# Kernel optimization log

Hardware: AMD Instinct MI355X
Metric: run time of the kernel (lower is better)

## Reference

```python
import jax, jax.numpy as jnp
import numpy as np

FG_THRESH = 0.5
BG_THRESH_HI = 0.5
BG_THRESH_LO = 0.1


def _bbox_overlaps(boxes, query):
    x1 = jnp.maximum(boxes[:, None, 0], query[None, :, 0])
    y1 = jnp.maximum(boxes[:, None, 1], query[None, :, 1])
    x2 = jnp.minimum(boxes[:, None, 2], query[None, :, 2])
    y2 = jnp.minimum(boxes[:, None, 3], query[None, :, 3])
    iw = jnp.clip(x2 - x1 + 1.0, 0.0)
    ih = jnp.clip(y2 - y1 + 1.0, 0.0)
    inter = iw * ih  # [N,C]
    area_b = (boxes[:, 2] - boxes[:, 0] + 1.0) * (boxes[:, 3] - boxes[:, 1] + 1.0)
    area_q = (query[:, 2] - query[:, 0] + 1.0) * (query[:, 3] - query[:, 1] + 1.0)
    return inter / (area_b[:, None] + area_q[None, :] - inter)


def _refine_supervision(prob, ss_boxes, pos_mask, IS_weight):
    # vectorized, fully on-device version of get_refine_supervision
    C = pos_mask.shape[0]
    p = jax.lax.stop_gradient(prob * IS_weight)  # original detaches via .data.cpu().numpy()
    if p.shape[1] == C + 1:
        p = p[:, 1:]  # drop background column
    max_idx = jnp.argmax(p, axis=0)                     # [C] top-scoring roi per class
    boxes_c = jax.lax.stop_gradient(ss_boxes)[max_idx, 1:5]  # [C,4] pseudo-GT boxes
    ov = _bbox_overlaps(jax.lax.stop_gradient(ss_boxes)[:, 1:5], boxes_c)  # [N,C]
    ov = jnp.where(pos_mask[None, :], ov, -1.0)         # only image-level positive classes
    gt = jnp.argmax(ov, axis=1)                         # [N] assignment
    mo = jnp.max(ov, axis=1)                            # [N] max overlap
    fg = mo > FG_THRESH
    bg = (mo >= BG_THRESH_LO) & (mo < BG_THRESH_HI)
    keep = fg | bg                                      # keep_inds as a mask
    col = jnp.where(fg, gt + 1, 0)                      # one-hot column per kept roi
    return keep, col


def _refine_loss(refine_prob, keep, col, IS_weight):
    n = jnp.sum(keep).astype(refine_prob.dtype)
    lp = jnp.take_along_axis(jnp.log(refine_prob), col[:, None], axis=1)[:, 0]  # [N]
    return -jnp.sum(jnp.where(keep, IS_weight[:, 0] * lp, 0.0)) / n


def reference(fc7_roi, fc7_context, fc7_frame, W_cls, b_cls, W_det, b_det,
              W_r1, b_r1, W_r2, b_r2, ss_boxes, IS_weight, image_level_label):
    C = W_cls.shape[1]
    cls_score = fc7_roi @ W_cls + b_cls                       # [N,C]
    det_score = (fc7_frame @ W_det + b_det) - (fc7_context @ W_det + b_det)  # frame - context
    refine_prob_1 = jax.nn.softmax(fc7_roi @ W_r1 + b_r1, axis=1)  # [N,C+1]
    refine_prob_2 = jax.nn.softmax(fc7_roi @ W_r2 + b_r2, axis=1)
    cls_prob = jax.nn.softmax(cls_score, axis=1)
    det_prob = jax.nn.softmax(det_score, axis=0)              # softmax over rois
    det_cls_prob_product = cls_prob * det_prob                # [N,C]
    det_cls_score = jnp.sum(cls_score * det_prob, axis=0)     # [C]

    pos_mask = image_level_label[0] == 1                      # [C]
    keep1, col1 = _refine_supervision(det_cls_prob_product, ss_boxes, pos_mask, IS_weight)
    refine_loss_1 = _refine_loss(refine_prob_1, keep1, col1, IS_weight)
    keep2, col2 = _refine_supervision(refine_prob_1, ss_boxes, pos_mask, IS_weight)
    refine_loss_2 = _refine_loss(refine_prob_2, keep2, col2, IS_weight)

    lab = image_level_label[0].astype(det_cls_score.dtype)    # +/-1 labels
    cls_det_loss = jnp.sum(jnp.maximum(0.0, 1.0 - lab * det_cls_score)) / C
    total_loss = cls_det_loss + 0.1 * refine_loss_1 + 0.1 * refine_loss_2
    return total_loss


def setup_inputs() -> dict:
    key = jax.random.key(0)
    ks = jax.random.split(key, 16)
    N, F, C = 4096, 4096, 20
    s = 0.01  # weight scale to keep softmax/hinge well-conditioned
    fc7_roi = jax.random.normal(ks[0], (N, F), jnp.float32)
    fc7_context = jax.random.normal(ks[1], (N, F), jnp.float32)
    fc7_frame = jax.random.normal(ks[2], (N, F), jnp.float32)
    W_cls = jax.random.normal(ks[3], (F, C), jnp.float32) * s
    W_det = jax.random.normal(ks[4], (F, C), jnp.float32) * s
    W_r1 = jax.random.normal(ks[5], (F, C + 1), jnp.float32) * s
    W_r2 = jax.random.normal(ks[6], (F, C + 1), jnp.float32) * s
    b_cls = jnp.zeros((C,), jnp.float32)
    b_det = jnp.zeros((C,), jnp.float32)
    b_r1 = jnp.zeros((C + 1,), jnp.float32)
    b_r2 = jnp.zeros((C + 1,), jnp.float32)
    x1 = jax.random.uniform(ks[7], (N,), jnp.float32, 0.0, 500.0)
    y1 = jax.random.uniform(ks[8], (N,), jnp.float32, 0.0, 500.0)
    w = jax.random.uniform(ks[9], (N,), jnp.float32, 10.0, 120.0)
    h = jax.random.uniform(ks[10], (N,), jnp.float32, 10.0, 120.0)
    ss_boxes = jnp.stack([jnp.zeros((N,), jnp.float32), x1, y1, x1 + w, y1 + h], axis=1)
    IS_weight = jax.random.uniform(ks[11], (N, 1), jnp.float32, 0.5, 1.0)
    lbl = jnp.where(jax.random.bernoulli(ks[12], 0.4, (1, C)), 1, -1).astype(jnp.int32)
    lbl = lbl.at[0, 0].set(1)  # guarantee at least one positive class
    return {"fc7_roi": fc7_roi, "fc7_context": fc7_context, "fc7_frame": fc7_frame,
            "W_cls": W_cls, "b_cls": b_cls, "W_det": W_det, "b_det": b_det,
            "W_r1": W_r1, "b_r1": b_r1, "W_r2": W_r2, "b_r2": b_r2,
            "ss_boxes": ss_boxes, "IS_weight": IS_weight, "image_level_label": lbl}
```

## Files before the change

### kernel.cpp

```cpp
#include <hip/hip_runtime.h>

typedef __attribute__((ext_vector_type(4))) float f32x4;
typedef __attribute__((ext_vector_type(8))) short short8;

#define N_ROWS 4096
#define KDIM   4096
#define NC     96
#define NSPLIT 16

__device__ inline short f2bf(float f) {
  unsigned u = __builtin_bit_cast(unsigned, f);
  u += 0x7FFFu + ((u >> 16) & 1u);
  return (short)(u >> 16);
}

__global__ void k_pack(const float* __restrict__ Wcls, const float* __restrict__ Wr1,
                       const float* __restrict__ Wr2, const float* __restrict__ Wdet,
                       ushort* __restrict__ Wp) {
  int t = blockIdx.x * 256 + threadIdx.x;
  int ks = t / 3072;
  int rem = t - ks * 3072;
  int ct = rem >> 9;
  int rem2 = rem & 511;
  int l = rem2 >> 3;
  int j = rem2 & 7;
  int k = ks * 32 + (l >> 4) * 8 + j;
  int col = ct * 16 + (l & 15);
  float v = 0.f;
  if (col < 20)                 v = Wcls[k * 20 + col];
  else if (col < 41)            v = Wr1[k * 21 + (col - 20)];
  else if (col < 62)            v = Wr2[k * 21 + (col - 41)];
  else if (col >= 64 && col < 84) v = Wdet[k * 20 + (col - 64)];
  Wp[t] = (ushort)f2bf(v);
}

__global__ __launch_bounds__(256) void k_gemm(const float* __restrict__ roi,
    const float* __restrict__ frame, const float* __restrict__ ctx,
    const ushort* __restrict__ Wp, float* __restrict__ Spart) {
  const int lane = threadIdx.x & 63;
  const int wid = blockIdx.x * 4 + (threadIdx.x >> 6);
  const int rt = wid & 255;
  const int ks = wid >> 8;
  const int row = rt * 16 + (lane & 15);
  const int kg = lane >> 4;
  const float* pr = roi   + (size_t)row * KDIM;
  const float* pf = frame + (size_t)row * KDIM;
  const float* pc = ctx   + (size_t)row * KDIM;
  f32x4 acc[6];
#pragma unroll
  for (int i = 0; i < 6; ++i) acc[i] = (f32x4){0.f, 0.f, 0.f, 0.f};
  const int s0 = ks * 8;
  for (int s = 0; s < 8; ++s) {
    const int kk = (s0 + s) * 32 + kg * 8;
    f32x4 r0 = *(const f32x4*)(pr + kk);
    f32x4 r1 = *(const f32x4*)(pr + kk + 4);
    f32x4 f0 = *(const f32x4*)(pf + kk);
    f32x4 f1 = *(const f32x4*)(pf + kk + 4);
    f32x4 c0 = *(const f32x4*)(pc + kk);
    f32x4 c1 = *(const f32x4*)(pc + kk + 4);
    short8 aR, aD;
#pragma unroll
    for (int j = 0; j < 4; ++j) {
      aR[j]     = f2bf(r0[j]);
      aR[j + 4] = f2bf(r1[j]);
      aD[j]     = f2bf(f0[j] - c0[j]);
      aD[j + 4] = f2bf(f1[j] - c1[j]);
    }
    const ushort* wb = Wp + ((size_t)(s0 + s) * 6) * 512 + lane * 8;
#pragma unroll
    for (int ct = 0; ct < 6; ++ct) {
      short8 b = *(const short8*)(wb + ct * 512);
      acc[ct] = __builtin_amdgcn_mfma_f32_16x16x32_bf16(ct < 4 ? aR : aD, b, acc[ct], 0, 0, 0);
    }
  }
  float* out = Spart + (size_t)ks * (N_ROWS * NC) + (size_t)rt * 16 * NC;
  const int rbase = (lane >> 4) * 4;
  const int col = lane & 15;
#pragma unroll
  for (int ct = 0; ct < 6; ++ct)
#pragma unroll
    for (int r = 0; r < 4; ++r)
      out[(size_t)(rbase + r) * NC + ct * 16 + col] = acc[ct][r];
}

__global__ void k_reduce(const float* __restrict__ Spart, float* __restrict__ S) {
  int e = blockIdx.x * 256 + threadIdx.x;
  float s = 0.f;
#pragma unroll
  for (int ks = 0; ks < NSPLIT; ++ks) s += Spart[(size_t)ks * (N_ROWS * NC) + e];
  S[e] = s;
}

__global__ void k_rows(const float* __restrict__ S, const float* __restrict__ bcls,
    const float* __restrict__ br1, const float* __restrict__ br2,
    float* __restrict__ clsp, float* __restrict__ rp1,
    float* __restrict__ lse1, float* __restrict__ lse2) {
  int i = blockIdx.x * 256 + threadIdx.x;
  const float* sr = S + (size_t)i * NC;
  float s[21];
  float m = -3.4e38f;
  for (int c = 0; c < 20; ++c) { s[c] = sr[c] + bcls[c]; m = fmaxf(m, s[c]); }
  float sum = 0.f;
  for (int c = 0; c < 20; ++c) { float e = expf(s[c] - m); s[c] = e; sum += e; }
  float inv = 1.f / sum;
  for (int c = 0; c < 20; ++c) clsp[(size_t)i * 20 + c] = s[c] * inv;
  m = -3.4e38f;
  for (int c = 0; c < 21; ++c) { s[c] = sr[20 + c] + br1[c]; m = fmaxf(m, s[c]); }
  sum = 0.f;
  for (int c = 0; c < 21; ++c) { float e = expf(s[c] - m); s[c] = e; sum += e; }
  lse1[i] = m + logf(sum);
  inv = 1.f / sum;
  for (int c = 0; c < 21; ++c) rp1[(size_t)i * 21 + c] = s[c] * inv;
  m = -3.4e38f;
  for (int c = 0; c < 21; ++c) { s[c] = sr[41 + c] + br2[c]; m = fmaxf(m, s[c]); }
  sum = 0.f;
  for (int c = 0; c < 21; ++c) sum += expf(s[c] - m);
  lse2[i] = m + logf(sum);
}

__global__ __launch_bounds__(256) void k_col(const float* __restrict__ S,
    const float* __restrict__ clsp, const float* __restrict__ rp1,
    const float* __restrict__ isw, const float* __restrict__ ssb,
    const float* __restrict__ bcls,
    float* __restrict__ dcs, float* __restrict__ b1out, float* __restrict__ b2out) {
  const int c = blockIdx.x;
  const int t = threadIdx.x;
  __shared__ float rv[256];
  __shared__ int ri[256];
  float m = -3.4e38f;
  for (int i = t; i < N_ROWS; i += 256) m = fmaxf(m, S[(size_t)i * NC + 64 + c]);
  rv[t] = m; __syncthreads();
  for (int o = 128; o; o >>= 1) { if (t < o) rv[t] = fmaxf(rv[t], rv[t + o]); __syncthreads(); }
  const float M = rv[0]; __syncthreads();
  float se = 0.f, scd = 0.f, v1b = -3.4e38f, v2b = -3.4e38f;
  int i1 = 0, i2 = 0;
  for (int i = t; i < N_ROWS; i += 256) {
    float w = isw[i];
    float e = expf(S[(size_t)i * NC + 64 + c] - M);
    se += e;
    scd += (S[(size_t)i * NC + c] + bcls[c]) * e;
    float v1 = clsp[(size_t)i * 20 + c] * e * w;
    if (v1 > v1b) { v1b = v1; i1 = i; }
    float v2 = rp1[(size_t)i * 21 + c + 1] * w;
    if (v2 > v2b) { v2b = v2; i2 = i; }
  }
  rv[t] = se; __syncthreads();
  for (int o = 128; o; o >>= 1) { if (t < o) rv[t] += rv[t + o]; __syncthreads(); }
  const float SE = rv[0]; __syncthreads();
  rv[t] = scd; __syncthreads();
  for (int o = 128; o; o >>= 1) { if (t < o) rv[t] += rv[t + o]; __syncthreads(); }
  const float SCD = rv[0]; __syncthreads();
  rv[t] = v1b; ri[t] = i1; __syncthreads();
  for (int o = 128; o; o >>= 1) {
    if (t < o) { if (rv[t + o] > rv[t] || (rv[t + o] == rv[t] && ri[t + o] < ri[t])) { rv[t] = rv[t + o]; ri[t] = ri[t + o]; } }
    __syncthreads();
  }
  const int I1 = ri[0]; __syncthreads();
  rv[t] = v2b; ri[t] = i2; __syncthreads();
  for (int o = 128; o; o >>= 1) {
    if (t < o) { if (rv[t + o] > rv[t] || (rv[t + o] == rv[t] && ri[t + o] < ri[t])) { rv[t] = rv[t + o]; ri[t] = ri[t + o]; } }
    __syncthreads();
  }
  const int I2 = ri[0];
  if (t == 0) {
    dcs[c] = SCD / SE;
    for (int q = 0; q < 4; ++q) {
      b1out[c * 4 + q] = ssb[(size_t)I1 * 5 + 1 + q];
      b2out[c * 4 + q] = ssb[(size_t)I2 * 5 + 1 + q];
    }
  }
}

__global__ __launch_bounds__(256) void k_sup(const float* __restrict__ S,
    const float* __restrict__ ssb, const float* __restrict__ isw,
    const int* __restrict__ label,
    const float* __restrict__ b1in, const float* __restrict__ b2in,
    const float* __restrict__ lse1, const float* __restrict__ lse2,
    const float* __restrict__ br1, const float* __restrict__ br2,
    float* __restrict__ scal) {
  __shared__ float q1[20][4], q2[20][4], a1[20], a2[20];
  __shared__ int pos[20];
  const int t = threadIdx.x;
  if (t < 20) {
    for (int q = 0; q < 4; ++q) { q1[t][q] = b1in[t * 4 + q]; q2[t][q] = b2in[t * 4 + q]; }
    a1[t] = (q1[t][2] - q1[t][0] + 1.f) * (q1[t][3] - q1[t][1] + 1.f);
    a2[t] = (q2[t][2] - q2[t][0] + 1.f) * (q2[t][3] - q2[t][1] + 1.f);
    pos[t] = (label[t] == 1);
  }
  __syncthreads();
  const int i = blockIdx.x * 256 + t;
  const float bx1 = ssb[(size_t)i * 5 + 1], by1 = ssb[(size_t)i * 5 + 2];
  const float bx2 = ssb[(size_t)i * 5 + 3], by2 = ssb[(size_t)i * 5 + 4];
  const float ab = (bx2 - bx1 + 1.f) * (by2 - by1 + 1.f);
  const float w = isw[i];
  float p1 = 0.f, n1 = 0.f, p2 = 0.f, n2 = 0.f;
  {
    float mo = -2.f; int gt = 0;
    for (int c = 0; c < 20; ++c) {
      float v = -1.f;
      if (pos[c]) {
        float xx1 = fmaxf(bx1, q1[c][0]), yy1 = fmaxf(by1, q1[c][1]);
        float xx2 = fminf(bx2, q1[c][2]), yy2 = fminf(by2, q1[c][3]);
        float iw = fmaxf(xx2 - xx1 + 1.f, 0.f), ih = fmaxf(yy2 - yy1 + 1.f, 0.f);
        float inter = iw * ih;
        v = inter / (ab + a1[c] - inter);
      }
      if (v > mo) { mo = v; gt = c; }
    }
    bool fg = mo > 0.5f;
    bool bg = (mo >= 0.1f) && (mo < 0.5f);
    if (fg || bg) {
      int col = fg ? gt + 1 : 0;
      float lp = S[(size_t)i * NC + 20 + col] + br1[col] - lse1[i];
      p1 = w * lp; n1 = 1.f;
    }
  }
  {
    float mo = -2.f; int gt = 0;
    for (int c = 0; c < 20; ++c) {
      float v = -1.f;
      if (pos[c]) {
        float xx1 = fmaxf(bx1, q2[c][0]), yy1 = fmaxf(by1, q2[c][1]);
        float xx2 = fminf(bx2, q2[c][2]), yy2 = fminf(by2, q2[c][3]);
        float iw = fmaxf(xx2 - xx1 + 1.f, 0.f), ih = fmaxf(yy2 - yy1 + 1.f, 0.f);
        float inter = iw * ih;
        v = inter / (ab + a2[c] - inter);
      }
      if (v > mo) { mo = v; gt = c; }
    }
    bool fg = mo > 0.5f;
    bool bg = (mo >= 0.1f) && (mo < 0.5f);
    if (fg || bg) {
      int col = fg ? gt + 1 : 0;
      float lp = S[(size_t)i * NC + 41 + col] + br2[col] - lse2[i];
      p2 = w * lp; n2 = 1.f;
    }
  }
  __shared__ float rs[256];
  float sums[4] = {p1, n1, p2, n2};
  float tot[4];
  for (int q = 0; q < 4; ++q) {
    rs[t] = sums[q]; __syncthreads();
    for (int o = 128; o; o >>= 1) { if (t < o) rs[t] += rs[t + o]; __syncthreads(); }
    tot[q] = rs[0]; __syncthreads();
  }
  if (t == 0) {
    atomicAdd(&scal[0], tot[0]); atomicAdd(&scal[1], tot[1]);
    atomicAdd(&scal[2], tot[2]); atomicAdd(&scal[3], tot[3]);
  }
}

__global__ void k_final(const float* __restrict__ dcs, const int* __restrict__ label,
                        const float* __restrict__ scal, float* __restrict__ out) {
  if (threadIdx.x == 0 && blockIdx.x == 0) {
    float cd = 0.f;
    for (int c = 0; c < 20; ++c) {
      float lab = (float)label[c];
      cd += fmaxf(1.f - lab * dcs[c], 0.f);
    }
    cd *= (1.f / 20.f);
    float rl1 = -scal[0] / scal[1];
    float rl2 = -scal[2] / scal[3];
    out[0] = cd + 0.1f * (rl1 + rl2);
  }
}

constexpr size_t OFF_S     = 0;
constexpr size_t OFF_SCAL  = OFF_S + (size_t)N_ROWS * NC * 4;
constexpr size_t OFF_DCS   = OFF_SCAL + 16;
constexpr size_t OFF_B1    = OFF_DCS + 80;
constexpr size_t OFF_B2    = OFF_B1 + 320;
constexpr size_t OFF_LSE1  = OFF_B2 + 320;
constexpr size_t OFF_LSE2  = OFF_LSE1 + 16384;
constexpr size_t OFF_CLSP  = OFF_LSE2 + 16384;
constexpr size_t OFF_RP1   = OFF_CLSP + 327680;
constexpr size_t OFF_WP    = OFF_RP1 + 344064;
constexpr size_t OFF_SPART = OFF_WP + 786432;

extern "C" void kernel_launch(void* const* d_in, const int* in_sizes, int n_in,
                              void* d_out, int out_size, void* d_ws, size_t ws_size,
                              hipStream_t stream) {
  const float* roi   = (const float*)d_in[0];
  const float* ctx   = (const float*)d_in[1];
  const float* frame = (const float*)d_in[2];
  const float* Wcls  = (const float*)d_in[3];
  const float* bcls  = (const float*)d_in[4];
  const float* Wdet  = (const float*)d_in[5];
  const float* Wr1   = (const float*)d_in[7];
  const float* br1   = (const float*)d_in[8];
  const float* Wr2   = (const float*)d_in[9];
  const float* br2   = (const float*)d_in[10];
  const float* ssb   = (const float*)d_in[11];
  const float* isw   = (const float*)d_in[12];
  const int*   label = (const int*)d_in[13];

  char* ws = (char*)d_ws;
  float*  S     = (float*)(ws + OFF_S);
  float*  scal  = (float*)(ws + OFF_SCAL);
  float*  dcs   = (float*)(ws + OFF_DCS);
  float*  b1    = (float*)(ws + OFF_B1);
  float*  b2    = (float*)(ws + OFF_B2);
  float*  lse1  = (float*)(ws + OFF_LSE1);
  float*  lse2  = (float*)(ws + OFF_LSE2);
  float*  clsp  = (float*)(ws + OFF_CLSP);
  float*  rp1   = (float*)(ws + OFF_RP1);
  ushort* Wp    = (ushort*)(ws + OFF_WP);
  float*  Spart = (float*)(ws + OFF_SPART);

  hipMemsetAsync(scal, 0, 16, stream);
  k_pack<<<1536, 256, 0, stream>>>(Wcls, Wr1, Wr2, Wdet, Wp);
  k_gemm<<<1024, 256, 0, stream>>>(roi, frame, ctx, Wp, Spart);
  k_reduce<<<1536, 256, 0, stream>>>(Spart, S);
  k_rows<<<16, 256, 0, stream>>>(S, bcls, br1, br2, clsp, rp1, lse1, lse2);
  k_col<<<20, 256, 0, stream>>>(S, clsp, rp1, isw, ssb, bcls, dcs, b1, b2);
  k_sup<<<16, 256, 0, stream>>>(S, ssb, isw, label, b1, b2, lse1, lse2, br1, br2, scal);
  k_final<<<1, 64, 0, stream>>>(dcs, label, scal, (float*)d_out);
}
```

Measured before the change: 96.03 us.

## Pipeline GEMM A loads with triple buffering, stage B in LDS, fuse reduce+rows

```diff
diff --git a/kernel.cpp b/kernel.cpp
--- a/kernel.cpp
+++ b/kernel.cpp
@@ -2,11 +2,12 @@
 
 typedef __attribute__((ext_vector_type(4))) float f32x4;
 typedef __attribute__((ext_vector_type(8))) short short8;
+typedef __attribute__((ext_vector_type(4))) unsigned int u32x4;
 
 #define N_ROWS 4096
 #define KDIM   4096
 #define NC     96
-#define NSPLIT 16
+#define GSPLIT 16
 
 __device__ inline short f2bf(float f) {
   unsigned u = __builtin_bit_cast(unsigned, f);
@@ -14,17 +15,23 @@
   return (short)(u >> 16);
 }
 
+__device__ inline unsigned cvtpk(float lo, float hi) {
+  unsigned r;
+  asm("v_cvt_pk_bf16_f32 %0, %1, %2" : "=v"(r) : "v"(lo), "v"(hi));
+  return r;
+}
+
 __global__ void k_pack(const float* __restrict__ Wcls, const float* __restrict__ Wr1,
                        const float* __restrict__ Wr2, const float* __restrict__ Wdet,
                        ushort* __restrict__ Wp) {
   int t = blockIdx.x * 256 + threadIdx.x;
-  int ks = t / 3072;
-  int rem = t - ks * 3072;
+  int K = t / 3072;
+  int rem = t - K * 3072;
   int ct = rem >> 9;
   int rem2 = rem & 511;
   int l = rem2 >> 3;
   int j = rem2 & 7;
-  int k = ks * 32 + (l >> 4) * 8 + j;
+  int k = K * 32 + (l >> 4) * 8 + j;
   int col = ct * 16 + (l & 15);
   float v = 0.f;
   if (col < 20)                 v = Wcls[k * 20 + col];
@@ -34,46 +41,79 @@
   Wp[t] = (ushort)f2bf(v);
 }
 
-__global__ __launch_bounds__(256) void k_gemm(const float* __restrict__ roi,
+#define GLo(dst, base, OFF) \
+  asm volatile("global_load_dwordx4 %0, %1, off offset:%c2" : "=v"(dst) : "v"(base), "i"(OFF) : "memory")
+#define WAITV(N) asm volatile("s_waitcnt vmcnt(" #N ")" ::: "memory")
+#define SB() __builtin_amdgcn_sched_barrier(0)
+
+#define ISSUEA(KS, BF) do {                              \
+    GLo(raw[BF][0], pr, (KS)*128);                       \
+    GLo(raw[BF][1], pr, (KS)*128 + 16);                  \
+    GLo(raw[BF][2], pf, (KS)*128);                       \
+    GLo(raw[BF][3], pf, (KS)*128 + 16);                  \
+    GLo(raw[BF][4], pc, (KS)*128);                       \
+    GLo(raw[BF][5], pc, (KS)*128 + 16);                  \
+  } while (0)
+
+__global__ __launch_bounds__(256, 3) void k_gemm(const float* __restrict__ roi,
     const float* __restrict__ frame, const float* __restrict__ ctx,
     const ushort* __restrict__ Wp, float* __restrict__ Spart) {
-  const int lane = threadIdx.x & 63;
-  const int wid = blockIdx.x * 4 + (threadIdx.x >> 6);
-  const int rt = wid & 255;
-  const int ks = wid >> 8;
-  const int row = rt * 16 + (lane & 15);
-  const int kg = lane >> 4;
-  const float* pr = roi   + (size_t)row * KDIM;
-  const float* pf = frame + (size_t)row * KDIM;
-  const float* pc = ctx   + (size_t)row * KDIM;
+  const int t    = threadIdx.x;
+  const int lane = t & 63;
+  const int wid  = t >> 6;
+  const int rb   = blockIdx.x >> 4;
+  const int g    = blockIdx.x & 15;
+
+  __shared__ alignas(16) ushort smemB[8 * 6 * 64 * 8];
+
+  {
+    const ushort* src = Wp + (size_t)g * 24576;
+    for (int r = 0; r < 12; ++r) {
+      const int e = r * 256 + t;
+      *(short8*)(&smemB[e * 8]) = *(const short8*)(src + e * 8);
+    }
+  }
+  __syncthreads();
+
+  const int row = rb * 64 + wid * 16 + (lane & 15);
+  const size_t aoff = (size_t)row * KDIM + g * 256 + (lane >> 4) * 8;
+  const float* pr = roi   + aoff;
+  const float* pf = frame + aoff;
+  const float* pc = ctx   + aoff;
+
+  f32x4 raw[3][6];
   f32x4 acc[6];
 #pragma unroll
   for (int i = 0; i < 6; ++i) acc[i] = (f32x4){0.f, 0.f, 0.f, 0.f};
-  const int s0 = ks * 8;
-  for (int s = 0; s < 8; ++s) {
-    const int kk = (s0 + s) * 32 + kg * 8;
-    f32x4 r0 = *(const f32x4*)(pr + kk);
-    f32x4 r1 = *(const f32x4*)(pr + kk + 4);
-    f32x4 f0 = *(const f32x4*)(pf + kk);
-    f32x4 f1 = *(const f32x4*)(pf + kk + 4);
-    f32x4 c0 = *(const f32x4*)(pc + kk);
-    f32x4 c1 = *(const f32x4*)(pc + kk + 4);
-    short8 aR, aD;
-#pragma unroll
-    for (int j = 0; j < 4; ++j) {
-      aR[j]     = f2bf(r0[j]);
-      aR[j + 4] = f2bf(r1[j]);
-      aD[j]     = f2bf(f0[j] - c0[j]);
-      aD[j + 4] = f2bf(f1[j] - c1[j]);
-    }
-    const ushort* wb = Wp + ((size_t)(s0 + s) * 6) * 512 + lane * 8;
+
+  ISSUEA(0, 0);
+  ISSUEA(1, 1);
+
+#pragma unroll
+  for (int ks = 0; ks < 8; ++ks) {
+    if (ks < 6) ISSUEA(ks + 2, (ks + 2) % 3);
+    if (ks < 6)      { WAITV(12); }
+    else if (ks == 6){ WAITV(6); }
+    else             { WAITV(0); }
+    SB();
+    const f32x4* c = raw[ks % 3];
+    u32x4 uR, uD;
+    uR.x = cvtpk(c[0][0], c[0][1]); uR.y = cvtpk(c[0][2], c[0][3]);
+    uR.z = cvtpk(c[1][0], c[1][1]); uR.w = cvtpk(c[1][2], c[1][3]);
+    uD.x = cvtpk(c[2][0] - c[4][0], c[2][1] - c[4][1]);
+    uD.y = cvtpk(c[2][2] - c[4][2], c[2][3] - c[4][3]);
+    uD.z = cvtpk(c[3][0] - c[5][0], c[3][1] - c[5][1]);
+    uD.w = cvtpk(c[3][2] - c[5][2], c[3][3] - c[5][3]);
+    const short8 aR = __builtin_bit_cast(short8, uR);
+    const short8 aD = __builtin_bit_cast(short8, uD);
 #pragma unroll
     for (int ct = 0; ct < 6; ++ct) {
-      short8 b = *(const short8*)(wb + ct * 512);
+      const short8 b = *(const short8*)(&smemB[((ks * 6 + ct) * 64 + lane) * 8]);
       acc[ct] = __builtin_amdgcn_mfma_f32_16x16x32_bf16(ct < 4 ? aR : aD, b, acc[ct], 0, 0, 0);
     }
   }
-  float* out = Spart + (size_t)ks * (N_ROWS * NC) + (size_t)rt * 16 * NC;
+
+  float* out = Spart + (size_t)g * (N_ROWS * NC) + (size_t)(rb * 64 + wid * 16) * NC;
   const int rbase = (lane >> 4) * 4;
   const int col = lane & 15;
 #pragma unroll
@@ -83,39 +123,45 @@
       out[(size_t)(rbase + r) * NC + ct * 16 + col] = acc[ct][r];
 }
 
-__global__ void k_reduce(const float* __restrict__ Spart, float* __restrict__ S) {
-  int e = blockIdx.x * 256 + threadIdx.x;
-  float s = 0.f;
-#pragma unroll
-  for (int ks = 0; ks < NSPLIT; ++ks) s += Spart[(size_t)ks * (N_ROWS * NC) + e];
-  S[e] = s;
-}
-
-__global__ void k_rows(const float* __restrict__ S, const float* __restrict__ bcls,
+__global__ void k_rr(const float* __restrict__ Spart, const float* __restrict__ bcls,
     const float* __restrict__ br1, const float* __restrict__ br2,
-    float* __restrict__ clsp, float* __restrict__ rp1,
+    float* __restrict__ S, float* __restrict__ clsp, float* __restrict__ rp1,
     float* __restrict__ lse1, float* __restrict__ lse2) {
-  int i = blockIdx.x * 256 + threadIdx.x;
-  const float* sr = S + (size_t)i * NC;
-  float s[21];
-  float m = -3.4e38f;
-  for (int c = 0; c < 20; ++c) { s[c] = sr[c] + bcls[c]; m = fmaxf(m, s[c]); }
-  float sum = 0.f;
-  for (int c = 0; c < 20; ++c) { float e = expf(s[c] - m); s[c] = e; sum += e; }
-  float inv = 1.f / sum;
-  for (int c = 0; c < 20; ++c) clsp[(size_t)i * 20 + c] = s[c] * inv;
-  m = -3.4e38f;
-  for (int c = 0; c < 21; ++c) { s[c] = sr[20 + c] + br1[c]; m = fmaxf(m, s[c]); }
-  sum = 0.f;
-  for (int c = 0; c < 21; ++c) { float e = expf(s[c] - m); s[c] = e; sum += e; }
-  lse1[i] = m + logf(sum);
-  inv = 1.f / sum;
-  for (int c = 0; c < 21; ++c) rp1[(size_t)i * 21 + c] = s[c] * inv;
-  m = -3.4e38f;
-  for (int c = 0; c < 21; ++c) { s[c] = sr[41 + c] + br2[c]; m = fmaxf(m, s[c]); }
-  sum = 0.f;
-  for (int c = 0; c < 21; ++c) sum += expf(s[c] - m);
-  lse2[i] = m + logf(sum);
+  const int b = blockIdx.x;
+  const int t = threadIdx.x;
+  const int base = b * 3072;
+#pragma unroll
+  for (int j = 0; j < 12; ++j) {
+    const int e = base + j * 256 + t;
+    float s = 0.f;
+#pragma unroll
+    for (int gg = 0; gg < GSPLIT; ++gg) s += Spart[(size_t)gg * (N_ROWS * NC) + e];
+    S[e] = s;
+  }
+  __syncthreads();
+  if (t < 32) {
+    const int i = b * 32 + t;
+    const float* sr = S + (size_t)i * NC;
+    float s[21];
+    float m = -3.4e38f;
+    for (int c = 0; c < 20; ++c) { s[c] = sr[c] + bcls[c]; m = fmaxf(m, s[c]); }
+    float sum = 0.f;
+    for (int c = 0; c < 20; ++c) { float e = expf(s[c] - m); s[c] = e; sum += e; }
+    float inv = 1.f / sum;
+    for (int c = 0; c < 20; ++c) clsp[(size_t)i * 20 + c] = s[c] * inv;
+    m = -3.4e38f;
+    for (int c = 0; c < 21; ++c) { s[c] = sr[20 + c] + br1[c]; m = fmaxf(m, s[c]); }
+    sum = 0.f;
+    for (int c = 0; c < 21; ++c) { float e = expf(s[c] - m); s[c] = e; sum += e; }
+    lse1[i] = m + logf(sum);
+    inv = 1.f / sum;
+    for (int c = 0; c < 21; ++c) rp1[(size_t)i * 21 + c] = s[c] * inv;
+    m = -3.4e38f;
+    for (int c = 0; c < 21; ++c) { s[c] = sr[41 + c] + br2[c]; m = fmaxf(m, s[c]); }
+    sum = 0.f;
+    for (int c = 0; c < 21; ++c) sum += expf(s[c] - m);
+    lse2[i] = m + logf(sum);
+  }
 }
 
 __global__ __launch_bounds__(256) void k_col(const float* __restrict__ S,
@@ -310,8 +356,7 @@
   hipMemsetAsync(scal, 0, 16, stream);
   k_pack<<<1536, 256, 0, stream>>>(Wcls, Wr1, Wr2, Wdet, Wp);
   k_gemm<<<1024, 256, 0, stream>>>(roi, frame, ctx, Wp, Spart);
-  k_reduce<<<1536, 256, 0, stream>>>(Spart, S);
-  k_rows<<<16, 256, 0, stream>>>(S, bcls, br1, br2, clsp, rp1, lse1, lse2);
+  k_rr<<<128, 256, 0, stream>>>(Spart, bcls, br1, br2, S, clsp, rp1, lse1, lse2);
   k_col<<<20, 256, 0, stream>>>(S, clsp, rp1, isw, ssb, bcls, dcs, b1, b2);
   k_sup<<<16, 256, 0, stream>>>(S, ssb, isw, label, b1, b2, lse1, lse2, br1, br2, scal);
   k_final<<<1, 64, 0, stream>>>(dcs, label, scal, (float*)d_out);
```

New measurement: 90.72 us. 5.5% less time.
